# Kernel optimization log

Hardware: AMD Instinct MI355X
Metric: run time of the kernel (lower is better)

The kernel has to match this reference:

```python
import jax, jax.numpy as jnp
import numpy as np

DIM = 64  # per-head dim, matches init kwarg `dim`
SCALE = 1.0 / np.sqrt(DIM).astype(np.float32)


def setup_inputs() -> dict:
    key = jax.random.key(0)
    k1, k2, k3 = jax.random.split(key, 3)
    shape = (4, 16, 2048, DIM)  # [B, H, S, d]
    return {
        "q": jax.random.normal(k1, shape, dtype=jnp.float32),
        "k": jax.random.normal(k2, shape, dtype=jnp.float32),
        "v": jax.random.normal(k3, shape, dtype=jnp.float32),
    }


def reference(q, k, v):
    # attn = softmax(q @ k^T * scale) @ v  (dropout p=0.0 -> identity)
    scores = jnp.einsum("bhqd,bhkd->bhqk", q, k) * SCALE  # [B,H,S,S]
    attn = jax.nn.softmax(scores, axis=-1)
    return jnp.einsum("bhqk,bhkd->bhqd", attn, v)
```

## Files before the change

### kernel.cpp

```cpp
#include <hip/hip_runtime.h>
#include <hip/hip_bf16.h>

typedef __attribute__((ext_vector_type(8))) short bf16x8;
typedef __attribute__((ext_vector_type(16))) float f32x16;
typedef __attribute__((ext_vector_type(4))) float f32x4;
typedef __attribute__((ext_vector_type(2))) float f32x2;
typedef __attribute__((ext_vector_type(4))) unsigned short us4;
typedef __attribute__((ext_vector_type(8))) unsigned short us8;
typedef __attribute__((ext_vector_type(4))) unsigned int u32x4;

#define SEQ   2048
#define HDIM  64
#define QBLK  256
#define KVBLK 64
#define NT    (SEQ / KVBLK)
#define NBH   64

#if __has_builtin(__builtin_amdgcn_exp2f)
#define EXP2(x) __builtin_amdgcn_exp2f(x)
#else
#define EXP2(x) exp2f(x)
#endif
#define QSCALE 0.18033688011112042f

typedef const __attribute__((address_space(1))) unsigned int* gptr_t;
typedef __attribute__((address_space(3))) unsigned int* lptr_t;

__device__ inline unsigned short f2bf(float f) {
    return __builtin_bit_cast(unsigned short, __float2bfloat16(f));
}
__device__ inline unsigned packbf2(float a, float b) {
    const float2 p = make_float2(a, b);
    const __hip_bfloat162 h = __float22bfloat162_rn(p);
    unsigned r;
    __builtin_memcpy(&r, &h, 4);
    return r;
}

#define VCH 128
__global__ __launch_bounds__(256) void prep_kv(const float* __restrict__ K,
                                               const float* __restrict__ V,
                                               unsigned short* __restrict__ Kb,
                                               unsigned short* __restrict__ VT) {
    __shared__ unsigned short T[HDIM][VCH + 4];
    const int t   = threadIdx.x;
    const int bh  = blockIdx.y;
    const int kv0 = blockIdx.x * VCH;

    {
        const float* Ks = K + (size_t)bh * SEQ * HDIM + (size_t)kv0 * HDIM;
        unsigned short* Ko = Kb + (size_t)bh * SEQ * HDIM + (size_t)kv0 * HDIM;
        #pragma unroll
        for (int i = 0; i < 4; ++i) {
            const size_t e = ((size_t)(i * 256 + t)) * 8;
            const f32x4 a = *(const f32x4*)(Ks + e);
            const f32x4 b = *(const f32x4*)(Ks + e + 4);
            us8 h;
            #pragma unroll
            for (int j = 0; j < 4; ++j) { h[j] = f2bf(a[j]); h[4 + j] = f2bf(b[j]); }
            *(us8*)(Ko + e) = h;
        }
    }

    const float* Vb = V + (size_t)bh * SEQ * HDIM + (size_t)kv0 * HDIM;
    #pragma unroll
    for (int i = 0; i < 8; ++i) {
        const int idx = i * 256 + t;
        const int kv  = idx >> 4;
        const int d4  = idx & 15;
        const f32x4 v = *(const f32x4*)(Vb + (size_t)kv * HDIM + d4 * 4);
        #pragma unroll
        for (int j = 0; j < 4; ++j) T[d4 * 4 + j][kv] = f2bf(v[j]);
    }
    __syncthreads();
    unsigned short* Ob = VT + (size_t)bh * SEQ * HDIM + kv0;
    #pragma unroll
    for (int i = 0; i < 8; ++i) {
        const int o    = i * 256 + t;
        const int d    = o >> 5;
        const int slot = o & 31;
        const us4 h = *(const us4*)(&T[d][slot * 4]);
        *(us4*)(Ob + (size_t)d * SEQ + slot * 4) = h;
    }
}

__global__ __launch_bounds__(512, 4) void attn_fwd(
    const float* __restrict__ Q, const unsigned short* __restrict__ Kb,
    const unsigned short* __restrict__ VTb, float* __restrict__ O)
{
    __shared__ unsigned short K_lds[4][KVBLK * HDIM];
    __shared__ unsigned short VT_lds[4][HDIM * KVBLK];

    const int tid  = threadIdx.x;
    const int lane = tid & 63;
    const int wid  = tid >> 6;
    const int l31  = lane & 31;
    const int hi   = lane >> 5;

    const int id    = blockIdx.x;
    const int xcd   = id & 7;
    const int slot  = id >> 3;
    const int qtile = slot & 7;
    const int bh    = xcd * 8 + (slot >> 3);

    const float*          Qb  = Q   + (size_t)bh * SEQ * HDIM;
    const unsigned short* Kbh = Kb  + (size_t)bh * SEQ * HDIM;
    const unsigned short* Vbh = VTb + (size_t)bh * SEQ * HDIM;
    float*                Ob  = O   + (size_t)bh * SEQ * HDIM;

    const int lr = lane >> 3;
    const int lx = ((lane & 7) ^ lr) << 4;

    bf16x8 qfrag[4];
    {
        const float* qp = Qb + (size_t)(qtile*QBLK + wid*32 + l31)*HDIM + 8*hi;
        #pragma unroll
        for (int kc = 0; kc < 4; ++kc) {
            const f32x4 a = *(const f32x4*)(qp + 16*kc);
            const f32x4 b = *(const f32x4*)(qp + 16*kc + 4);
            bf16x8 f;
            #pragma unroll
            for (int j = 0; j < 4; ++j) {
                f[j]   = (short)f2bf(a[j] * QSCALE);
                f[4+j] = (short)f2bf(b[j] * QSCALE);
            }
            qfrag[kc] = f;
        }
    }

    f32x16 acc0 = {}, acc1 = {};
    float l_run = 0.f;

    #define STAGE(T_, B_) do {                                                 \
        const char* Ks_ = (const char*)Kbh + (size_t)(T_) * 8192;              \
        const char* Vs_ = (const char*)Vbh + (size_t)(T_) * 128;               \
        const int row_ = wid * 8 + lr;                                         \
        __builtin_amdgcn_global_load_lds(                                      \
            (gptr_t)(Ks_ + row_ * 128 + lx),                                   \
            (lptr_t)((char*)K_lds + (B_) * 8192 + wid * 1024), 16, 0, 0);      \
        __builtin_amdgcn_global_load_lds(                                      \
            (gptr_t)(Vs_ + (size_t)row_ * (SEQ * 2) + lx),                     \
            (lptr_t)((char*)VT_lds + (B_) * 8192 + wid * 1024), 16, 0, 0);     \
    } while (0)

    auto compute_tile = [&](int buf) {
        const char* Kc = (const char*)K_lds + buf * 8192;
        const char* Vc = (const char*)VT_lds + buf * 8192;
        const int sw = (l31 & 7) << 4;

        f32x16 s0 = {}, s1 = {};
        __builtin_amdgcn_s_setprio(1);
        #pragma unroll
        for (int kc = 0; kc < 4; ++kc) {
            const bf16x8 kf0 = *(const bf16x8*)(Kc + l31*128      + (((2*kc+hi) << 4) ^ sw));
            s0 = __builtin_amdgcn_mfma_f32_32x32x16_bf16(kf0, qfrag[kc], s0, 0, 0, 0);
        }
        #pragma unroll
        for (int kc = 0; kc < 4; ++kc) {
            const bf16x8 kf1 = *(const bf16x8*)(Kc + (32+l31)*128 + (((2*kc+hi) << 4) ^ sw));
            s1 = __builtin_amdgcn_mfma_f32_32x32x16_bf16(kf1, qfrag[kc], s1, 0, 0, 0);
        }
        __builtin_amdgcn_s_setprio(0);

        f32x2 ts2 = {0.f, 0.f};
        unsigned W0[8], W1[8];
        #pragma unroll
        for (int m = 0; m < 8; ++m) {
            const float p0 = EXP2(s0[2*m]), p1 = EXP2(s0[2*m+1]);
            ts2 += (f32x2){p0, p1};
            W0[m] = packbf2(p0, p1);
        }
        #pragma unroll
        for (int m = 0; m < 8; ++m) {
            const float p0 = EXP2(s1[2*m]), p1 = EXP2(s1[2*m+1]);
            ts2 += (f32x2){p0, p1};
            W1[m] = packbf2(p0, p1);
        }
        l_run += ts2[0] + ts2[1];

        __builtin_amdgcn_s_setprio(1);
        #pragma unroll
        for (int c = 0; c < 4; ++c) {
            unsigned pw[4];
            #pragma unroll
            for (int p = 0; p < 2; ++p) {
                const int i0 = 4*(c&1) + p;
                const int i1 = i0 + 2;
                const unsigned w_lo = (c >> 1) ? W1[i0] : W0[i0];
                const unsigned w_hi = (c >> 1) ? W1[i1] : W0[i1];
                const unsigned keep = hi ? w_hi : w_lo;
                const unsigned expo = hi ? w_lo : w_hi;
                const unsigned swp  = (unsigned)__shfl_xor((int)expo, 32, 64);
                pw[p]     = hi ? swp  : keep;
                pw[2 + p] = hi ? keep : swp;
            }
            const bf16x8 pf = __builtin_bit_cast(bf16x8, (u32x4){pw[0], pw[1], pw[2], pw[3]});
            const bf16x8 vf0 = *(const bf16x8*)(Vc + l31*128      + (((2*c+hi) << 4) ^ sw));
            acc0 = __builtin_amdgcn_mfma_f32_32x32x16_bf16(vf0, pf, acc0, 0, 0, 0);
            const bf16x8 vf1 = *(const bf16x8*)(Vc + (32+l31)*128 + (((2*c+hi) << 4) ^ sw));
            acc1 = __builtin_amdgcn_mfma_f32_32x32x16_bf16(vf1, pf, acc1, 0, 0, 0);
        }
        __builtin_amdgcn_s_setprio(0);
    };

    STAGE(0, 0);
    STAGE(1, 1);
    asm volatile("s_waitcnt vmcnt(0)" ::: "memory");
    __builtin_amdgcn_s_barrier();

    for (int i = 0; i < NT / 2; ++i) {
        const int tt = 2 * i;
        const int pc = (i & 1) ? 2 : 0;
        const int ps = 2 - pc;
        if (tt + 2 < NT) { STAGE(tt + 2, ps); STAGE(tt + 3, ps + 1); }

        compute_tile(pc);
        compute_tile(pc + 1);

        if (tt + 2 < NT) {
            asm volatile("s_waitcnt vmcnt(0)" ::: "memory");
            __builtin_amdgcn_s_barrier();
        }
    }

    const float l_tot = l_run + __shfl_xor(l_run, 32, 64);
    const float inv = 1.0f / l_tot;
    float* op = Ob + (size_t)(qtile*QBLK + wid*32 + l31)*HDIM + 4*hi;
    #pragma unroll
    for (int g = 0; g < 4; ++g) {
        f32x4 o;
        o[0] = acc0[4*g]   * inv; o[1] = acc0[4*g+1] * inv;
        o[2] = acc0[4*g+2] * inv; o[3] = acc0[4*g+3] * inv;
        *(f32x4*)(op + 8*g) = o;
        f32x4 o2;
        o2[0] = acc1[4*g]   * inv; o2[1] = acc1[4*g+1] * inv;
        o2[2] = acc1[4*g+2] * inv; o2[3] = acc1[4*g+3] * inv;
        *(f32x4*)(op + 32 + 8*g) = o2;
    }
    #undef STAGE
}

extern "C" void kernel_launch(void* const* d_in, const int* in_sizes, int n_in,
                              void* d_out, int out_size, void* d_ws, size_t ws_size,
                              hipStream_t stream) {
    const float* q = (const float*)d_in[0];
    const float* k = (const float*)d_in[1];
    const float* v = (const float*)d_in[2];
    float* o = (float*)d_out;

    unsigned short* Kb = (unsigned short*)d_ws;
    unsigned short* VT = (unsigned short*)((char*)d_ws + (size_t)NBH*SEQ*HDIM*2);

    prep_kv<<<dim3(SEQ / VCH, NBH), dim3(256), 0, stream>>>(k, v, Kb, VT);

    attn_fwd<<<dim3(512), dim3(512), 0, stream>>>(q, Kb, VT, o);
}
```

Before: 110.3 us.

## Software-pipeline QK of next tile with softmax-PV of current tile

Splits the per-tile work into a QK^T MFMA phase and a softmax/PV phase. The QK of tile t+1 is then issued before the exp/PV work of tile t, so matrix ops and transcendental work interleave. Loads now stage one tile at a time into a 4-slot LDS ring, with partial vmcnt waits in place of full drains. This aims to hide MFMA latency and load stalls, at the cost of holding two score accumulators live, which raises register pressure and risks lower occupancy.

```diff
diff --git a/kernel.cpp b/kernel.cpp
--- a/kernel.cpp
+++ b/kernel.cpp
@@ -22,6 +22,9 @@
 #define EXP2(x) exp2f(x)
 #endif
 #define QSCALE 0.18033688011112042f
+
+#define WAITVM2 asm volatile("s_waitcnt vmcnt(2)" ::: "memory")
+#define WAITVM0 asm volatile("s_waitcnt vmcnt(0)" ::: "memory")
 
 typedef const __attribute__((address_space(1))) unsigned int* gptr_t;
 typedef __attribute__((address_space(3))) unsigned int* lptr_t;
@@ -143,25 +146,24 @@
             (lptr_t)((char*)VT_lds + (B_) * 8192 + wid * 1024), 16, 0, 0);     \
     } while (0)
 
-    auto compute_tile = [&](int buf) {
+    const int sw = (l31 & 7) << 4;
+
+    auto QK = [&](int buf, f32x16& s0, f32x16& s1) {
         const char* Kc = (const char*)K_lds + buf * 8192;
-        const char* Vc = (const char*)VT_lds + buf * 8192;
-        const int sw = (l31 & 7) << 4;
-
-        f32x16 s0 = {}, s1 = {};
+        s0 = (f32x16){}; s1 = (f32x16){};
         __builtin_amdgcn_s_setprio(1);
         #pragma unroll
         for (int kc = 0; kc < 4; ++kc) {
             const bf16x8 kf0 = *(const bf16x8*)(Kc + l31*128      + (((2*kc+hi) << 4) ^ sw));
             s0 = __builtin_amdgcn_mfma_f32_32x32x16_bf16(kf0, qfrag[kc], s0, 0, 0, 0);
-        }
-        #pragma unroll
-        for (int kc = 0; kc < 4; ++kc) {
             const bf16x8 kf1 = *(const bf16x8*)(Kc + (32+l31)*128 + (((2*kc+hi) << 4) ^ sw));
             s1 = __builtin_amdgcn_mfma_f32_32x32x16_bf16(kf1, qfrag[kc], s1, 0, 0, 0);
         }
         __builtin_amdgcn_s_setprio(0);
-
+    };
+
+    auto PROC = [&](int buf, f32x16& s0, f32x16& s1) {
+        const char* Vc = (const char*)VT_lds + buf * 8192;
         f32x2 ts2 = {0.f, 0.f};
         unsigned W0[8], W1[8];
         #pragma unroll
@@ -203,25 +205,32 @@
         __builtin_amdgcn_s_setprio(0);
     };
 
+    f32x16 sA0, sA1, sB0, sB1;
+
     STAGE(0, 0);
     STAGE(1, 1);
-    asm volatile("s_waitcnt vmcnt(0)" ::: "memory");
+    WAITVM2;
     __builtin_amdgcn_s_barrier();
-
-    for (int i = 0; i < NT / 2; ++i) {
-        const int tt = 2 * i;
-        const int pc = (i & 1) ? 2 : 0;
-        const int ps = 2 - pc;
-        if (tt + 2 < NT) { STAGE(tt + 2, ps); STAGE(tt + 3, ps + 1); }
-
-        compute_tile(pc);
-        compute_tile(pc + 1);
-
-        if (tt + 2 < NT) {
-            asm volatile("s_waitcnt vmcnt(0)" ::: "memory");
-            __builtin_amdgcn_s_barrier();
-        }
-    }
+    QK(0, sA0, sA1);
+
+    for (int t = 1; t + 1 < NT; t += 2) {
+        STAGE(t + 1, (t + 1) & 3);
+        WAITVM2;
+        __builtin_amdgcn_s_barrier();
+        QK(t & 3, sB0, sB1);
+        PROC((t - 1) & 3, sA0, sA1);
+
+        if (t + 2 < NT) { STAGE(t + 2, (t + 2) & 3); WAITVM2; }
+        else            { WAITVM0; }
+        __builtin_amdgcn_s_barrier();
+        QK((t + 1) & 3, sA0, sA1);
+        PROC(t & 3, sB0, sB1);
+    }
+    WAITVM0;
+    __builtin_amdgcn_s_barrier();
+    QK((NT - 1) & 3, sB0, sB1);
+    PROC((NT - 2) & 3, sA0, sA1);
+    PROC((NT - 1) & 3, sB0, sB1);
 
     const float l_tot = l_run + __shfl_xor(l_run, 32, 64);
     const float inv = 1.0f / l_tot;
```

Measured after the change: 129.5 us. +17.4%, slower.
